# Kernel optimization log

Hardware: AMD Instinct MI355X
Metric: run time of the kernel (lower is better)

## Reference

```python
import jax, jax.numpy as jnp
import numpy as np

N = 512      # num_neurons
D = 32       # delay_dim
T = 8192     # number of sequential timesteps
OMEGA = 10.0 # base_freq
ALPHA = 0.5
DT = 1e-3    # dt_global per tick
TWO_PI = float(2.0 * np.pi)


def setup_inputs() -> dict:
    key = jax.random.key(0)
    k = jax.random.split(key, 6)
    X_real = jax.random.normal(k[0], (T, D), jnp.float32)
    X_imag = jax.random.normal(k[1], (T, D), jnp.float32)
    target_wave = jax.random.normal(k[2], (T,), jnp.float32)
    # W initialized as torch.polar(rand*0.1, rand*2pi)
    mag = jax.random.uniform(k[3], (N, D), jnp.float32) * 0.1
    ang = jax.random.uniform(k[4], (N, D), jnp.float32) * TWO_PI
    W_real = mag * jnp.cos(ang)
    W_imag = mag * jnp.sin(ang)
    phi0 = jax.random.uniform(k[5], (N,), jnp.float32) * TWO_PI
    beta0 = jnp.linspace(0.005, 0.05, N, dtype=jnp.float32)
    return {"X_real": X_real, "X_imag": X_imag, "target_wave": target_wave,
            "W_real": W_real, "W_imag": W_imag, "phi0": phi0, "beta0": beta0}


def _run(X_real, X_imag, target_wave, W_real, W_imag, phi0, beta0):
    W0 = (W_real + 1j * W_imag).astype(jnp.complex64)   # [N, D]
    X = (X_real + 1j * X_imag).astype(jnp.complex64)    # [T, D]
    lt0 = jnp.zeros((N,), jnp.float32)                  # local_time
    err0 = jnp.float32(0.0)                             # err_smooth

    def step(carry, inp):
        W, phi, beta, lt, err = carry
        x, tgt = inp                                    # x: [D] complex, tgt: scalar
        gamma = jnp.exp(-ALPHA * beta)                  # time dilation Γ  [N]
        dt_local = gamma * DT                           # [N]
        lt = lt + dt_local
        Z = W @ x                                       # X_c @ W.T -> [N] complex
        theta = OMEGA * lt + phi                        # [N]
        gate = jax.nn.relu(jnp.cos(theta - jnp.angle(Z)))
        Y = jnp.abs(Z) * gate                           # [N] real
        out = jnp.sum(Y * jnp.cos(theta))               # Re(sum Y * exp(i theta))
        # thermodynamic error feedback (sequential dependency)
        raw_err = jnp.abs(tgt - out)
        err = 0.99 * err + 0.01 * raw_err
        rel_err = err / (jnp.abs(tgt) + 0.01)
        beta_target = 3.5 * jnp.exp(-5.0 * rel_err)
        tau = jnp.where(beta_target > beta, 0.5 / (gamma + 1e-6), 0.03)
        a_s = 1.0 - jnp.exp(-DT / tau)
        beta_new = jnp.clip(beta + a_s * (beta_target - beta), 0.005, 5.0)
        # Hebbian growth / viscous decay (growth.T and decay.T directly in [N,D])
        growth_t = 0.05 * Y[:, None] * x[None, :]                 # [N, D] complex
        decay_t = (beta_new * Y ** 2)[:, None].astype(jnp.complex64) * W
        W = W + (growth_t - decay_t) * dt_local[:, None].astype(jnp.complex64)
        # phase pull: imag(tgt * exp(-i theta)) = -tgt*sin(theta) for real tgt
        phi = jnp.mod(phi + (2.0 / N) * (-tgt * jnp.sin(theta)) * dt_local, TWO_PI)
        return (W, phi, beta_new, lt, err), (out, beta_new, gamma)

    _, (outs, betas, gammas) = jax.lax.scan(
        step, (W0, phi0, beta0, lt0, err0), (X, target_wave))
    return outs, betas, gammas


def reference(X_real, X_imag, target_wave, W_real, W_imag, phi0, beta0):
    return _run(X_real, X_imag, target_wave, W_real, W_imag, phi0, beta0)
```

## Files before the change

### kernel.cpp

```cpp
#include <hip/hip_runtime.h>

#define NN 512
#define DD 32
#define TT 8192

typedef float v4f __attribute__((ext_vector_type(4)));
typedef __attribute__((address_space(3))) float lds_f;
typedef __attribute__((address_space(3))) void lds_v;
typedef const __attribute__((address_space(1))) void glb_v;

constexpr float F_OMEGA = 10.0f;
constexpr float F_DT = 1e-3f;
constexpr float F_TWO_PI = 6.28318530717958647692f;
constexpr float F_INV_TWO_PI = 0.15915494309189533577f;

__device__ __forceinline__ void barrier_lgkm() {
    asm volatile("s_waitcnt lgkmcnt(0)\n\ts_barrier" ::: "memory");
}

__device__ __forceinline__ void glds4(const float* g, lds_f* dst) {
    __builtin_amdgcn_global_load_lds((glb_v*)g, (lds_v*)dst, 4, 0, 0);
}

#define DSR128(dst, addr, off) \
    asm volatile("ds_read_b128 %0, %1 offset:" #off : "=v"(dst) : "v"(addr))
#define DSR32(dst, addr, off) \
    asm volatile("ds_read_b32 %0, %1 offset:" #off : "=v"(dst) : "v"(addr))

#define DPP_ADD(x, ctrl, rmask)                                                 \
    {                                                                           \
        int _t = __builtin_amdgcn_update_dpp(0, __float_as_int(x),              \
                                             (ctrl), (rmask), 0xf, true);       \
        (x) += __int_as_float(_t);                                              \
    }

__device__ __forceinline__ float wave_reduce_to_lane63(float x) {
    DPP_ADD(x, 0xB1, 0xf);
    DPP_ADD(x, 0x4E, 0xf);
    DPP_ADD(x, 0x141, 0xf);
    DPP_ADD(x, 0x140, 0xf);
    DPP_ADD(x, 0x142, 0xa);
    DPP_ADD(x, 0x143, 0xc);
    return x;
}

__device__ __forceinline__ float hsum4(v4f a) {
    return (a.x + a.y) + (a.z + a.w);
}

__global__ __launch_bounds__(512, 2) void deerskin(
    const float* __restrict__ Xr, const float* __restrict__ Xi,
    const float* __restrict__ Tg,
    const float* __restrict__ W0r, const float* __restrict__ W0i,
    const float* __restrict__ Phi0, const float* __restrict__ Beta0,
    float* __restrict__ outs, float* __restrict__ betas, float* __restrict__ gammas)
{
    __shared__ __align__(16) float xbuf[3][72];
    __shared__ __align__(16) float sP[16];

    const int n = threadIdx.x;
    const int lane = n & 63;
    const int wid = n >> 6;

    v4f wr4[8], wi4[8];
    {
        const v4f* wr0 = (const v4f*)(W0r + n * DD);
        const v4f* wi0 = (const v4f*)(W0i + n * DD);
#pragma unroll
        for (int j = 0; j < 8; ++j) { wr4[j] = wr0[j]; wi4[j] = wi0[j]; }
    }
    float phi = Phi0[n];
    float beta = Beta0[n];
    float lt = 0.0f;
    float err = 0.0f;

    const float* xsrc = ((lane < 32) ? Xr : Xi) + (lane & 31);

    lds_f* pcur = (lds_f*)&xbuf[0][0];
    lds_f* pnxt = (lds_f*)&xbuf[1][0];
    lds_f* pfut = (lds_f*)&xbuf[2][0];

    if (wid == 0) {
        glds4(xsrc, pcur);
        glds4(xsrc + DD, pnxt);
        if (lane == 0) {
            glds4(Tg, pcur + 64);
            glds4(Tg + 1, pnxt + 64);
        }
        asm volatile("s_waitcnt vmcnt(0)" ::: "memory");
    }
    barrier_lgkm();

    for (int t = 0; t < TT; ++t) {
        if (wid == 0) {
            int tf = t + 2; tf = (tf < TT) ? tf : (TT - 1);
            glds4(xsrc + (size_t)tf * DD, pfut);
            if (lane == 0) glds4(Tg + tf, pfut + 64);
        }

        const float gamma = __expf(-0.5f * beta);
        const float dtl = gamma * F_DT;
        lt += dtl;
        const float theta = fmaf(F_OMEGA, lt, phi);
        float rev = theta * F_INV_TWO_PI;
        rev -= floorf(rev);
        const float s = __builtin_amdgcn_sinf(rev);
        const float c = __builtin_amdgcn_cosf(rev);
        const float a_sA = 1.0f - __expf(-2.0f * F_DT * (gamma + 1e-6f));
        const float a_sB = 1.0f - __expf(-F_DT / 0.03f);

        const unsigned lcur = (unsigned)(unsigned long long)pcur;
        v4f cr[8], ci[8];
        float tgt;
        DSR128(cr[0], lcur, 0);   DSR128(cr[1], lcur, 16);
        DSR128(cr[2], lcur, 32);  DSR128(cr[3], lcur, 48);
        DSR128(cr[4], lcur, 64);  DSR128(cr[5], lcur, 80);
        DSR128(cr[6], lcur, 96);  DSR128(cr[7], lcur, 112);
        DSR128(ci[0], lcur, 128); DSR128(ci[1], lcur, 144);
        DSR128(ci[2], lcur, 160); DSR128(ci[3], lcur, 176);
        DSR128(ci[4], lcur, 192); DSR128(ci[5], lcur, 208);
        DSR128(ci[6], lcur, 224); DSR128(ci[7], lcur, 240);
        DSR32(tgt, lcur, 256);
        asm volatile("s_waitcnt lgkmcnt(0)"
            : "+v"(cr[0]), "+v"(cr[1]), "+v"(cr[2]), "+v"(cr[3]),
              "+v"(cr[4]), "+v"(cr[5]), "+v"(cr[6]), "+v"(cr[7]),
              "+v"(ci[0]), "+v"(ci[1]), "+v"(ci[2]), "+v"(ci[3]),
              "+v"(ci[4]), "+v"(ci[5]), "+v"(ci[6]), "+v"(ci[7]),
              "+v"(tgt) :: "memory");

        v4f Arr = {0,0,0,0}, Aii = {0,0,0,0}, Ari = {0,0,0,0}, Air = {0,0,0,0};
#pragma unroll
        for (int j = 0; j < 8; ++j) {
            Arr += wr4[j] * cr[j];
            Aii += wi4[j] * ci[j];
            Ari += wr4[j] * ci[j];
            Air += wi4[j] * cr[j];
        }
        const float zr = hsum4(Arr) - hsum4(Aii);
        const float zi = hsum4(Ari) + hsum4(Air);

        const float Y = fmaxf(fmaf(zr, c, zi * s), 0.0f);

        float v = wave_reduce_to_lane63(Y * c);
        if (lane == 63) sP[((t & 1) << 3) + wid] = v;

        const float inv_t = 1.0f / (fabsf(tgt) + 0.01f);
        const float yy = Y * Y;
        const float g = 0.05f * Y * dtl;
        phi += (2.0f / (float)NN) * (-tgt * s) * dtl;
        phi = phi - F_TWO_PI * floorf(phi * F_INV_TWO_PI);

        if (wid == 0) asm volatile("s_waitcnt vmcnt(5)" ::: "memory");
        barrier_lgkm();

        const float4* sp4 = (const float4*)(sP + ((t & 1) << 3));
        const float4 p0 = sp4[0], p1 = sp4[1];
        const float out = ((p0.x + p0.y) + (p0.z + p0.w)) +
                          ((p1.x + p1.y) + (p1.z + p1.w));

        const float raw = fabsf(tgt - out);
        err = 0.99f * err + 0.01f * raw;
        const float rel = err * inv_t;
        const float btg = 3.5f * __expf(-5.0f * rel);
        const float a_s = (btg > beta) ? a_sA : a_sB;
        float bnew = beta + a_s * (btg - beta);
        bnew = fminf(fmaxf(bnew, 0.005f), 5.0f);

        const float k = (bnew * yy) * dtl;
        const float m1 = 1.0f - k;
        const v4f m1v = {m1, m1, m1, m1};
        const v4f gv = {g, g, g, g};
#pragma unroll
        for (int j = 0; j < 8; ++j) {
            wr4[j] = wr4[j] * m1v + gv * cr[j];
            wi4[j] = wi4[j] * m1v + gv * ci[j];
        }

        gammas[t * NN + n] = gamma;
        betas[t * NN + n] = bnew;
        if (lane == 63) outs[t] = out;
        beta = bnew;

        lds_f* tmp = pcur; pcur = pnxt; pnxt = pfut; pfut = tmp;
    }
}

extern "C" void kernel_launch(void* const* d_in, const int* in_sizes, int n_in,
                              void* d_out, int out_size, void* d_ws, size_t ws_size,
                              hipStream_t stream) {
    const float* Xr    = (const float*)d_in[0];
    const float* Xi    = (const float*)d_in[1];
    const float* Tg    = (const float*)d_in[2];
    const float* W0r   = (const float*)d_in[3];
    const float* W0i   = (const float*)d_in[4];
    const float* Phi0  = (const float*)d_in[5];
    const float* Beta0 = (const float*)d_in[6];

    float* outs   = (float*)d_out;
    float* betas  = outs + TT;
    float* gammas = betas + (size_t)TT * NN;

    deerskin<<<1, NN, 0, stream>>>(Xr, Xi, Tg, W0r, W0i, Phi0, Beta0,
                                   outs, betas, gammas);
}
```

Measured before the change: 9.200 ms.

## Split each neuron's dot product across two threads using 1024-thread block

Each neuron is now handled by a thread pair, each owning half of the 32 delay weights, and partial complex sums are combined with a DPP swap. This halves the per-thread serial FMA chain and register footprint, and gives more waves per SIMD in the single-block sequential loop. In exchange, the per-step barrier spans 16 waves and extra reduction work is added. Scalar state (phi, beta, err) is computed redundantly on both threads of each pair.

```diff
diff --git a/kernel.cpp b/kernel.cpp
--- a/kernel.cpp
+++ b/kernel.cpp
@@ -48,7 +48,7 @@
     return (a.x + a.y) + (a.z + a.w);
 }
 
-__global__ __launch_bounds__(512, 2) void deerskin(
+__global__ __launch_bounds__(1024, 4) void deerskin(
     const float* __restrict__ Xr, const float* __restrict__ Xi,
     const float* __restrict__ Tg,
     const float* __restrict__ W0r, const float* __restrict__ W0i,
@@ -56,18 +56,20 @@
     float* __restrict__ outs, float* __restrict__ betas, float* __restrict__ gammas)
 {
     __shared__ __align__(16) float xbuf[3][72];
-    __shared__ __align__(16) float sP[16];
-
-    const int n = threadIdx.x;
-    const int lane = n & 63;
-    const int wid = n >> 6;
-
-    v4f wr4[8], wi4[8];
+    __shared__ __align__(16) float sP[32];
+
+    const int tid = threadIdx.x;
+    const int n = tid >> 1;
+    const int h = tid & 1;
+    const int lane = tid & 63;
+    const int wid = tid >> 6;
+
+    v4f wr4[4], wi4[4];
     {
-        const v4f* wr0 = (const v4f*)(W0r + n * DD);
-        const v4f* wi0 = (const v4f*)(W0i + n * DD);
+        const v4f* wr0 = (const v4f*)(W0r + n * DD + h * 16);
+        const v4f* wi0 = (const v4f*)(W0i + n * DD + h * 16);
 #pragma unroll
-        for (int j = 0; j < 8; ++j) { wr4[j] = wr0[j]; wi4[j] = wi0[j]; }
+        for (int j = 0; j < 4; ++j) { wr4[j] = wr0[j]; wi4[j] = wi0[j]; }
     }
     float phi = Phi0[n];
     float beta = Beta0[n];
@@ -110,39 +112,37 @@
         const float a_sB = 1.0f - __expf(-F_DT / 0.03f);
 
         const unsigned lcur = (unsigned)(unsigned long long)pcur;
-        v4f cr[8], ci[8];
+        const unsigned lhalf = lcur + (unsigned)(h * 64);
+        v4f cr[4], ci[4];
         float tgt;
-        DSR128(cr[0], lcur, 0);   DSR128(cr[1], lcur, 16);
-        DSR128(cr[2], lcur, 32);  DSR128(cr[3], lcur, 48);
-        DSR128(cr[4], lcur, 64);  DSR128(cr[5], lcur, 80);
-        DSR128(cr[6], lcur, 96);  DSR128(cr[7], lcur, 112);
-        DSR128(ci[0], lcur, 128); DSR128(ci[1], lcur, 144);
-        DSR128(ci[2], lcur, 160); DSR128(ci[3], lcur, 176);
-        DSR128(ci[4], lcur, 192); DSR128(ci[5], lcur, 208);
-        DSR128(ci[6], lcur, 224); DSR128(ci[7], lcur, 240);
+        DSR128(cr[0], lhalf, 0);   DSR128(cr[1], lhalf, 16);
+        DSR128(cr[2], lhalf, 32);  DSR128(cr[3], lhalf, 48);
+        DSR128(ci[0], lhalf, 128); DSR128(ci[1], lhalf, 144);
+        DSR128(ci[2], lhalf, 160); DSR128(ci[3], lhalf, 176);
         DSR32(tgt, lcur, 256);
         asm volatile("s_waitcnt lgkmcnt(0)"
             : "+v"(cr[0]), "+v"(cr[1]), "+v"(cr[2]), "+v"(cr[3]),
-              "+v"(cr[4]), "+v"(cr[5]), "+v"(cr[6]), "+v"(cr[7]),
               "+v"(ci[0]), "+v"(ci[1]), "+v"(ci[2]), "+v"(ci[3]),
-              "+v"(ci[4]), "+v"(ci[5]), "+v"(ci[6]), "+v"(ci[7]),
               "+v"(tgt) :: "memory");
 
         v4f Arr = {0,0,0,0}, Aii = {0,0,0,0}, Ari = {0,0,0,0}, Air = {0,0,0,0};
 #pragma unroll
-        for (int j = 0; j < 8; ++j) {
+        for (int j = 0; j < 4; ++j) {
             Arr += wr4[j] * cr[j];
             Aii += wi4[j] * ci[j];
             Ari += wr4[j] * ci[j];
             Air += wi4[j] * cr[j];
         }
-        const float zr = hsum4(Arr) - hsum4(Aii);
-        const float zi = hsum4(Ari) + hsum4(Air);
+        float zr = hsum4(Arr) - hsum4(Aii);
+        float zi = hsum4(Ari) + hsum4(Air);
+        DPP_ADD(zr, 0xB1, 0xf);
+        DPP_ADD(zi, 0xB1, 0xf);
 
         const float Y = fmaxf(fmaf(zr, c, zi * s), 0.0f);
 
-        float v = wave_reduce_to_lane63(Y * c);
-        if (lane == 63) sP[((t & 1) << 3) + wid] = v;
+        float v = h ? 0.0f : (Y * c);
+        v = wave_reduce_to_lane63(v);
+        if (lane == 63) sP[((t & 1) << 4) + wid] = v;
 
         const float inv_t = 1.0f / (fabsf(tgt) + 0.01f);
         const float yy = Y * Y;
@@ -153,10 +153,13 @@
         if (wid == 0) asm volatile("s_waitcnt vmcnt(5)" ::: "memory");
         barrier_lgkm();
 
-        const float4* sp4 = (const float4*)(sP + ((t & 1) << 3));
-        const float4 p0 = sp4[0], p1 = sp4[1];
-        const float out = ((p0.x + p0.y) + (p0.z + p0.w)) +
+        const float4* sp4 = (const float4*)(sP + ((t & 1) << 4));
+        const float4 p0 = sp4[0], p1 = sp4[1], p2 = sp4[2], p3 = sp4[3];
+        const float o01 = ((p0.x + p0.y) + (p0.z + p0.w)) +
                           ((p1.x + p1.y) + (p1.z + p1.w));
+        const float o23 = ((p2.x + p2.y) + (p2.z + p2.w)) +
+                          ((p3.x + p3.y) + (p3.z + p3.w));
+        const float out = o01 + o23;
 
         const float raw = fabsf(tgt - out);
         err = 0.99f * err + 0.01f * raw;
@@ -171,13 +174,15 @@
         const v4f m1v = {m1, m1, m1, m1};
         const v4f gv = {g, g, g, g};
 #pragma unroll
-        for (int j = 0; j < 8; ++j) {
+        for (int j = 0; j < 4; ++j) {
             wr4[j] = wr4[j] * m1v + gv * cr[j];
             wi4[j] = wi4[j] * m1v + gv * ci[j];
         }
 
-        gammas[t * NN + n] = gamma;
-        betas[t * NN + n] = bnew;
+        if (h == 0) {
+            gammas[t * NN + n] = gamma;
+            betas[t * NN + n] = bnew;
+        }
         if (lane == 63) outs[t] = out;
         beta = bnew;
 
@@ -200,6 +205,6 @@
     float* betas  = outs + TT;
     float* gammas = betas + (size_t)TT * NN;
 
-    deerskin<<<1, NN, 0, stream>>>(Xr, Xi, Tg, W0r, W0i, Phi0, Beta0,
-                                   outs, betas, gammas);
-}
+    deerskin<<<1, 1024, 0, stream>>>(Xr, Xi, Tg, W0r, W0i, Phi0, Beta0,
+                                     outs, betas, gammas);
+}
```

Result: slower. 11.54 ms (+25.4%).

## Load x rows directly into registers with one-step-ahead global prefetch

Applied to the files above, without the earlier changes.

Drops the LDS staging ring, where wave 0 copied each row of x and the target into LDS and every thread then read it back with ds_read. Each thread now issues broadcast global_load_dwordx4 loads for the next timestep straight into a second register set. The loop is unrolled by two so the two register sets swap roles each step. This removes the LDS round trip and wave 0's vmcnt wait ahead of the barrier. In exchange every wave issues 17 vector memory loads per step, doubles the register footprint for x, and depends on a hand-counted vmcnt(21) that assumes a fixed number of stores are in flight.

```diff
diff --git a/kernel.cpp b/kernel.cpp
--- a/kernel.cpp
+++ b/kernel.cpp
@@ -5,9 +5,6 @@
 #define TT 8192
 
 typedef float v4f __attribute__((ext_vector_type(4)));
-typedef __attribute__((address_space(3))) float lds_f;
-typedef __attribute__((address_space(3))) void lds_v;
-typedef const __attribute__((address_space(1))) void glb_v;
 
 constexpr float F_OMEGA = 10.0f;
 constexpr float F_DT = 1e-3f;
@@ -18,14 +15,14 @@
     asm volatile("s_waitcnt lgkmcnt(0)\n\ts_barrier" ::: "memory");
 }
 
-__device__ __forceinline__ void glds4(const float* g, lds_f* dst) {
-    __builtin_amdgcn_global_load_lds((glb_v*)g, (lds_v*)dst, 4, 0, 0);
-}
-
-#define DSR128(dst, addr, off) \
-    asm volatile("ds_read_b128 %0, %1 offset:" #off : "=v"(dst) : "v"(addr))
-#define DSR32(dst, addr, off) \
-    asm volatile("ds_read_b32 %0, %1 offset:" #off : "=v"(dst) : "v"(addr))
+#define GLD4M(dst, base, off) \
+    asm volatile("global_load_dwordx4 %0, %1, off offset:" #off \
+                 : "=v"(dst) : "v"(base) : "memory")
+#define GLD4(dst, base, off) \
+    asm volatile("global_load_dwordx4 %0, %1, off offset:" #off \
+                 : "=v"(dst) : "v"(base))
+#define GLD1(dst, base) \
+    asm volatile("global_load_dword %0, %1, off" : "=v"(dst) : "v"(base))
 
 #define DPP_ADD(x, ctrl, rmask)                                                 \
     {                                                                           \
@@ -48,6 +45,113 @@
     return (a.x + a.y) + (a.z + a.w);
 }
 
+__device__ __forceinline__ void issue_batch(
+    int tn, const float* Xr, const float* Xi, const float* Tg,
+    v4f (&nr)[8], v4f (&ni)[8], float& ntg)
+{
+    const unsigned long long bxr = (unsigned long long)(Xr + (size_t)tn * DD);
+    const unsigned long long bxi = (unsigned long long)(Xi + (size_t)tn * DD);
+    const unsigned long long btg = (unsigned long long)(Tg + tn);
+    GLD4M(nr[0], bxr, 0);   GLD4(nr[1], bxr, 16);
+    GLD4(nr[2], bxr, 32);   GLD4(nr[3], bxr, 48);
+    GLD4(nr[4], bxr, 64);   GLD4(nr[5], bxr, 80);
+    GLD4(nr[6], bxr, 96);   GLD4(nr[7], bxr, 112);
+    GLD4(ni[0], bxi, 0);    GLD4(ni[1], bxi, 16);
+    GLD4(ni[2], bxi, 32);   GLD4(ni[3], bxi, 48);
+    GLD4(ni[4], bxi, 64);   GLD4(ni[5], bxi, 80);
+    GLD4(ni[6], bxi, 96);   GLD4(ni[7], bxi, 112);
+    GLD1(ntg, btg);
+}
+
+#define WAIT_BATCH(cr, ci, tgt, cnt)                                            \
+    asm volatile("s_waitcnt vmcnt(" #cnt ")"                                    \
+        : "+v"(cr[0]), "+v"(cr[1]), "+v"(cr[2]), "+v"(cr[3]),                   \
+          "+v"(cr[4]), "+v"(cr[5]), "+v"(cr[6]), "+v"(cr[7]),                   \
+          "+v"(ci[0]), "+v"(ci[1]), "+v"(ci[2]), "+v"(ci[3]),                   \
+          "+v"(ci[4]), "+v"(ci[5]), "+v"(ci[6]), "+v"(ci[7]),                   \
+          "+v"(tgt) :: "memory")
+
+__device__ __forceinline__ void do_step(
+    int t,
+    const float* __restrict__ Xr, const float* __restrict__ Xi,
+    const float* __restrict__ Tg,
+    v4f (&wr4)[8], v4f (&wi4)[8],
+    v4f (&cr)[8], v4f (&ci)[8], float& tgt,
+    v4f (&nr)[8], v4f (&ni)[8], float& ntg,
+    float& phi, float& beta, float& lt, float& err,
+    float* __restrict__ outs, float* __restrict__ betas, float* __restrict__ gammas,
+    float* sP, int n, int lane, int wid)
+{
+    int tn = t + 1; tn = (tn < TT) ? tn : (TT - 1);
+    issue_batch(tn, Xr, Xi, Tg, nr, ni, ntg);
+
+    const float gamma = __expf(-0.5f * beta);
+    const float dtl = gamma * F_DT;
+    lt += dtl;
+    const float theta = fmaf(F_OMEGA, lt, phi);
+    float rev = theta * F_INV_TWO_PI;
+    rev -= floorf(rev);
+    const float s = __builtin_amdgcn_sinf(rev);
+    const float c = __builtin_amdgcn_cosf(rev);
+    const float a_sA = 1.0f - __expf(-2.0f * F_DT * (gamma + 1e-6f));
+    const float a_sB = 1.0f - __expf(-F_DT / 0.03f);
+
+    gammas[t * NN + n] = gamma;
+
+    WAIT_BATCH(cr, ci, tgt, 21);
+
+    v4f Arr = {0,0,0,0}, Aii = {0,0,0,0}, Ari = {0,0,0,0}, Air = {0,0,0,0};
+#pragma unroll
+    for (int j = 0; j < 8; ++j) {
+        Arr += wr4[j] * cr[j];
+        Aii += wi4[j] * ci[j];
+        Ari += wr4[j] * ci[j];
+        Air += wi4[j] * cr[j];
+    }
+    const float zr = hsum4(Arr) - hsum4(Aii);
+    const float zi = hsum4(Ari) + hsum4(Air);
+
+    const float Y = fmaxf(fmaf(zr, c, zi * s), 0.0f);
+
+    float v = wave_reduce_to_lane63(Y * c);
+    if (lane == 63) sP[((t & 1) << 3) + wid] = v;
+
+    const float inv_t = 1.0f / (fabsf(tgt) + 0.01f);
+    const float yy = Y * Y;
+    const float g = 0.05f * Y * dtl;
+    phi += (2.0f / (float)NN) * (-tgt * s) * dtl;
+    phi = phi - F_TWO_PI * floorf(phi * F_INV_TWO_PI);
+
+    barrier_lgkm();
+
+    const float4* sp4 = (const float4*)(sP + ((t & 1) << 3));
+    const float4 p0 = sp4[0], p1 = sp4[1];
+    const float out = ((p0.x + p0.y) + (p0.z + p0.w)) +
+                      ((p1.x + p1.y) + (p1.z + p1.w));
+
+    const float raw = fabsf(tgt - out);
+    err = 0.99f * err + 0.01f * raw;
+    const float rel = err * inv_t;
+    const float btg = 3.5f * __expf(-5.0f * rel);
+    const float a_s = (btg > beta) ? a_sA : a_sB;
+    float bnew = beta + a_s * (btg - beta);
+    bnew = fminf(fmaxf(bnew, 0.005f), 5.0f);
+
+    const float k = (bnew * yy) * dtl;
+    const float m1 = 1.0f - k;
+    const v4f m1v = {m1, m1, m1, m1};
+    const v4f gv = {g, g, g, g};
+#pragma unroll
+    for (int j = 0; j < 8; ++j) {
+        wr4[j] = wr4[j] * m1v + gv * cr[j];
+        wi4[j] = wi4[j] * m1v + gv * ci[j];
+    }
+
+    betas[t * NN + n] = bnew;
+    if (lane == 63) outs[t] = out;
+    beta = bnew;
+}
+
 __global__ __launch_bounds__(512, 2) void deerskin(
     const float* __restrict__ Xr, const float* __restrict__ Xi,
     const float* __restrict__ Tg,
@@ -55,7 +159,6 @@
     const float* __restrict__ Phi0, const float* __restrict__ Beta0,
     float* __restrict__ outs, float* __restrict__ betas, float* __restrict__ gammas)
 {
-    __shared__ __align__(16) float xbuf[3][72];
     __shared__ __align__(16) float sP[16];
 
     const int n = threadIdx.x;
@@ -74,114 +177,20 @@
     float lt = 0.0f;
     float err = 0.0f;
 
-    const float* xsrc = ((lane < 32) ? Xr : Xi) + (lane & 31);
-
-    lds_f* pcur = (lds_f*)&xbuf[0][0];
-    lds_f* pnxt = (lds_f*)&xbuf[1][0];
-    lds_f* pfut = (lds_f*)&xbuf[2][0];
-
-    if (wid == 0) {
-        glds4(xsrc, pcur);
-        glds4(xsrc + DD, pnxt);
-        if (lane == 0) {
-            glds4(Tg, pcur + 64);
-            glds4(Tg + 1, pnxt + 64);
-        }
-        asm volatile("s_waitcnt vmcnt(0)" ::: "memory");
-    }
+    v4f xa_r[8], xa_i[8], xb_r[8], xb_i[8];
+    float tgtA, tgtB;
+
+    issue_batch(0, Xr, Xi, Tg, xa_r, xa_i, tgtA);
+    WAIT_BATCH(xa_r, xa_i, tgtA, 0);
     barrier_lgkm();
 
-    for (int t = 0; t < TT; ++t) {
-        if (wid == 0) {
-            int tf = t + 2; tf = (tf < TT) ? tf : (TT - 1);
-            glds4(xsrc + (size_t)tf * DD, pfut);
-            if (lane == 0) glds4(Tg + tf, pfut + 64);
-        }
-
-        const float gamma = __expf(-0.5f * beta);
-        const float dtl = gamma * F_DT;
-        lt += dtl;
-        const float theta = fmaf(F_OMEGA, lt, phi);
-        float rev = theta * F_INV_TWO_PI;
-        rev -= floorf(rev);
-        const float s = __builtin_amdgcn_sinf(rev);
-        const float c = __builtin_amdgcn_cosf(rev);
-        const float a_sA = 1.0f - __expf(-2.0f * F_DT * (gamma + 1e-6f));
-        const float a_sB = 1.0f - __expf(-F_DT / 0.03f);
-
-        const unsigned lcur = (unsigned)(unsigned long long)pcur;
-        v4f cr[8], ci[8];
-        float tgt;
-        DSR128(cr[0], lcur, 0);   DSR128(cr[1], lcur, 16);
-        DSR128(cr[2], lcur, 32);  DSR128(cr[3], lcur, 48);
-        DSR128(cr[4], lcur, 64);  DSR128(cr[5], lcur, 80);
-        DSR128(cr[6], lcur, 96);  DSR128(cr[7], lcur, 112);
-        DSR128(ci[0], lcur, 128); DSR128(ci[1], lcur, 144);
-        DSR128(ci[2], lcur, 160); DSR128(ci[3], lcur, 176);
-        DSR128(ci[4], lcur, 192); DSR128(ci[5], lcur, 208);
-        DSR128(ci[6], lcur, 224); DSR128(ci[7], lcur, 240);
-        DSR32(tgt, lcur, 256);
-        asm volatile("s_waitcnt lgkmcnt(0)"
-            : "+v"(cr[0]), "+v"(cr[1]), "+v"(cr[2]), "+v"(cr[3]),
-              "+v"(cr[4]), "+v"(cr[5]), "+v"(cr[6]), "+v"(cr[7]),
-              "+v"(ci[0]), "+v"(ci[1]), "+v"(ci[2]), "+v"(ci[3]),
-              "+v"(ci[4]), "+v"(ci[5]), "+v"(ci[6]), "+v"(ci[7]),
-              "+v"(tgt) :: "memory");
-
-        v4f Arr = {0,0,0,0}, Aii = {0,0,0,0}, Ari = {0,0,0,0}, Air = {0,0,0,0};
-#pragma unroll
-        for (int j = 0; j < 8; ++j) {
-            Arr += wr4[j] * cr[j];
-            Aii += wi4[j] * ci[j];
-            Ari += wr4[j] * ci[j];
-            Air += wi4[j] * cr[j];
-        }
-        const float zr = hsum4(Arr) - hsum4(Aii);
-        const float zi = hsum4(Ari) + hsum4(Air);
-
-        const float Y = fmaxf(fmaf(zr, c, zi * s), 0.0f);
-
-        float v = wave_reduce_to_lane63(Y * c);
-        if (lane == 63) sP[((t & 1) << 3) + wid] = v;
-
-        const float inv_t = 1.0f / (fabsf(tgt) + 0.01f);
-        const float yy = Y * Y;
-        const float g = 0.05f * Y * dtl;
-        phi += (2.0f / (float)NN) * (-tgt * s) * dtl;
-        phi = phi - F_TWO_PI * floorf(phi * F_INV_TWO_PI);
-
-        if (wid == 0) asm volatile("s_waitcnt vmcnt(5)" ::: "memory");
-        barrier_lgkm();
-
-        const float4* sp4 = (const float4*)(sP + ((t & 1) << 3));
-        const float4 p0 = sp4[0], p1 = sp4[1];
-        const float out = ((p0.x + p0.y) + (p0.z + p0.w)) +
-                          ((p1.x + p1.y) + (p1.z + p1.w));
-
-        const float raw = fabsf(tgt - out);
-        err = 0.99f * err + 0.01f * raw;
-        const float rel = err * inv_t;
-        const float btg = 3.5f * __expf(-5.0f * rel);
-        const float a_s = (btg > beta) ? a_sA : a_sB;
-        float bnew = beta + a_s * (btg - beta);
-        bnew = fminf(fmaxf(bnew, 0.005f), 5.0f);
-
-        const float k = (bnew * yy) * dtl;
-        const float m1 = 1.0f - k;
-        const v4f m1v = {m1, m1, m1, m1};
-        const v4f gv = {g, g, g, g};
-#pragma unroll
-        for (int j = 0; j < 8; ++j) {
-            wr4[j] = wr4[j] * m1v + gv * cr[j];
-            wi4[j] = wi4[j] * m1v + gv * ci[j];
-        }
-
-        gammas[t * NN + n] = gamma;
-        betas[t * NN + n] = bnew;
-        if (lane == 63) outs[t] = out;
-        beta = bnew;
-
-        lds_f* tmp = pcur; pcur = pnxt; pnxt = pfut; pfut = tmp;
+    for (int t = 0; t < TT; t += 2) {
+        do_step(t,     Xr, Xi, Tg, wr4, wi4,
+                xa_r, xa_i, tgtA, xb_r, xb_i, tgtB,
+                phi, beta, lt, err, outs, betas, gammas, sP, n, lane, wid);
+        do_step(t + 1, Xr, Xi, Tg, wr4, wi4,
+                xb_r, xb_i, tgtB, xa_r, xa_i, tgtA,
+                phi, beta, lt, err, outs, betas, gammas, sP, n, lane, wid);
     }
 }
 
```

Result: slower. 12.15 ms (+32.1%).

## Load x once per lane and broadcast via readlane, prefetching next step

Applied to the files above, without the earlier changes.

Instead of every lane reading all 64 x values from LDS with 16 broadcast ds_read_b128 ops, each lane reads one value and the wave uses v_readlane into SGPRs to build the operand vectors. The next timestep's x and target are read right after the barrier, so the LDS latency overlaps with the error/beta update and W update. Math switches from v4f to v2f ops to suit packed-FMA with scalar operands. This cuts LDS bandwidth and VGPR pressure but adds 64 readlane instructions per step, which may serialize on the scalar path.

```diff
diff --git a/kernel.cpp b/kernel.cpp
--- a/kernel.cpp
+++ b/kernel.cpp
@@ -4,7 +4,7 @@
 #define DD 32
 #define TT 8192
 
-typedef float v4f __attribute__((ext_vector_type(4)));
+typedef float v2f __attribute__((ext_vector_type(2)));
 typedef __attribute__((address_space(3))) float lds_f;
 typedef __attribute__((address_space(3))) void lds_v;
 typedef const __attribute__((address_space(1))) void glb_v;
@@ -22,10 +22,10 @@
     __builtin_amdgcn_global_load_lds((glb_v*)g, (lds_v*)dst, 4, 0, 0);
 }
 
-#define DSR128(dst, addr, off) \
-    asm volatile("ds_read_b128 %0, %1 offset:" #off : "=v"(dst) : "v"(addr))
 #define DSR32(dst, addr, off) \
     asm volatile("ds_read_b32 %0, %1 offset:" #off : "=v"(dst) : "v"(addr))
+#define WAIT2(a, b) \
+    asm volatile("s_waitcnt lgkmcnt(0)" : "+v"(a), "+v"(b) :: "memory")
 
 #define DPP_ADD(x, ctrl, rmask)                                                 \
     {                                                                           \
@@ -44,8 +44,15 @@
     return x;
 }
 
-__device__ __forceinline__ float hsum4(v4f a) {
-    return (a.x + a.y) + (a.z + a.w);
+__device__ __forceinline__ void unpack_readlane(float vx, v2f (&xr)[16], v2f (&xi)[16]) {
+    const int vxi = __float_as_int(vx);
+#pragma unroll
+    for (int j = 0; j < 16; ++j) {
+        xr[j] = v2f{__int_as_float(__builtin_amdgcn_readlane(vxi, 2 * j)),
+                    __int_as_float(__builtin_amdgcn_readlane(vxi, 2 * j + 1))};
+        xi[j] = v2f{__int_as_float(__builtin_amdgcn_readlane(vxi, 32 + 2 * j)),
+                    __int_as_float(__builtin_amdgcn_readlane(vxi, 32 + 2 * j + 1))};
+    }
 }
 
 __global__ __launch_bounds__(512, 2) void deerskin(
@@ -62,12 +69,12 @@
     const int lane = n & 63;
     const int wid = n >> 6;
 
-    v4f wr4[8], wi4[8];
+    v2f wr[16], wi[16];
     {
-        const v4f* wr0 = (const v4f*)(W0r + n * DD);
-        const v4f* wi0 = (const v4f*)(W0i + n * DD);
-#pragma unroll
-        for (int j = 0; j < 8; ++j) { wr4[j] = wr0[j]; wi4[j] = wi0[j]; }
+        const v2f* wr0 = (const v2f*)(W0r + n * DD);
+        const v2f* wi0 = (const v2f*)(W0i + n * DD);
+#pragma unroll
+        for (int j = 0; j < 16; ++j) { wr[j] = wr0[j]; wi[j] = wi0[j]; }
     }
     float phi = Phi0[n];
     float beta = Beta0[n];
@@ -79,6 +86,9 @@
     lds_f* pcur = (lds_f*)&xbuf[0][0];
     lds_f* pnxt = (lds_f*)&xbuf[1][0];
     lds_f* pfut = (lds_f*)&xbuf[2][0];
+
+    v2f xr[16], xi[16];
+    float tgt;
 
     if (wid == 0) {
         glds4(xsrc, pcur);
@@ -90,6 +100,15 @@
         asm volatile("s_waitcnt vmcnt(0)" ::: "memory");
     }
     barrier_lgkm();
+    {
+        const unsigned lcur = (unsigned)(unsigned long long)pcur;
+        float vx, vtg;
+        DSR32(vx, lcur + 4u * (unsigned)lane, 0);
+        DSR32(vtg, lcur, 256);
+        WAIT2(vx, vtg);
+        unpack_readlane(vx, xr, xi);
+        tgt = vtg;
+    }
 
     for (int t = 0; t < TT; ++t) {
         if (wid == 0) {
@@ -109,35 +128,16 @@
         const float a_sA = 1.0f - __expf(-2.0f * F_DT * (gamma + 1e-6f));
         const float a_sB = 1.0f - __expf(-F_DT / 0.03f);
 
-        const unsigned lcur = (unsigned)(unsigned long long)pcur;
-        v4f cr[8], ci[8];
-        float tgt;
-        DSR128(cr[0], lcur, 0);   DSR128(cr[1], lcur, 16);
-        DSR128(cr[2], lcur, 32);  DSR128(cr[3], lcur, 48);
-        DSR128(cr[4], lcur, 64);  DSR128(cr[5], lcur, 80);
-        DSR128(cr[6], lcur, 96);  DSR128(cr[7], lcur, 112);
-        DSR128(ci[0], lcur, 128); DSR128(ci[1], lcur, 144);
-        DSR128(ci[2], lcur, 160); DSR128(ci[3], lcur, 176);
-        DSR128(ci[4], lcur, 192); DSR128(ci[5], lcur, 208);
-        DSR128(ci[6], lcur, 224); DSR128(ci[7], lcur, 240);
-        DSR32(tgt, lcur, 256);
-        asm volatile("s_waitcnt lgkmcnt(0)"
-            : "+v"(cr[0]), "+v"(cr[1]), "+v"(cr[2]), "+v"(cr[3]),
-              "+v"(cr[4]), "+v"(cr[5]), "+v"(cr[6]), "+v"(cr[7]),
-              "+v"(ci[0]), "+v"(ci[1]), "+v"(ci[2]), "+v"(ci[3]),
-              "+v"(ci[4]), "+v"(ci[5]), "+v"(ci[6]), "+v"(ci[7]),
-              "+v"(tgt) :: "memory");
-
-        v4f Arr = {0,0,0,0}, Aii = {0,0,0,0}, Ari = {0,0,0,0}, Air = {0,0,0,0};
-#pragma unroll
-        for (int j = 0; j < 8; ++j) {
-            Arr += wr4[j] * cr[j];
-            Aii += wi4[j] * ci[j];
-            Ari += wr4[j] * ci[j];
-            Air += wi4[j] * cr[j];
-        }
-        const float zr = hsum4(Arr) - hsum4(Aii);
-        const float zi = hsum4(Ari) + hsum4(Air);
+        v2f Arr = {0.f,0.f}, Aii = {0.f,0.f}, Ari = {0.f,0.f}, Air = {0.f,0.f};
+#pragma unroll
+        for (int j = 0; j < 16; ++j) {
+            Arr += wr[j] * xr[j];
+            Aii += wi[j] * xi[j];
+            Ari += wr[j] * xi[j];
+            Air += wi[j] * xr[j];
+        }
+        const float zr = (Arr.x + Arr.y) - (Aii.x + Aii.y);
+        const float zi = (Ari.x + Ari.y) + (Air.x + Air.y);
 
         const float Y = fmaxf(fmaf(zr, c, zi * s), 0.0f);
 
@@ -152,6 +152,13 @@
 
         if (wid == 0) asm volatile("s_waitcnt vmcnt(5)" ::: "memory");
         barrier_lgkm();
+
+        float vx, vtg;
+        {
+            const unsigned lnxt = (unsigned)(unsigned long long)pnxt;
+            DSR32(vx, lnxt + 4u * (unsigned)lane, 0);
+            DSR32(vtg, lnxt, 256);
+        }
 
         const float4* sp4 = (const float4*)(sP + ((t & 1) << 3));
         const float4 p0 = sp4[0], p1 = sp4[1];
@@ -168,18 +175,22 @@
 
         const float k = (bnew * yy) * dtl;
         const float m1 = 1.0f - k;
-        const v4f m1v = {m1, m1, m1, m1};
-        const v4f gv = {g, g, g, g};
-#pragma unroll
-        for (int j = 0; j < 8; ++j) {
-            wr4[j] = wr4[j] * m1v + gv * cr[j];
-            wi4[j] = wi4[j] * m1v + gv * ci[j];
+        const v2f m1v = {m1, m1};
+        const v2f gv = {g, g};
+#pragma unroll
+        for (int j = 0; j < 16; ++j) {
+            wr[j] = wr[j] * m1v + gv * xr[j];
+            wi[j] = wi[j] * m1v + gv * xi[j];
         }
 
         gammas[t * NN + n] = gamma;
         betas[t * NN + n] = bnew;
         if (lane == 63) outs[t] = out;
         beta = bnew;
+
+        WAIT2(vx, vtg);
+        unpack_readlane(vx, xr, xi);
+        tgt = vtg;
 
         lds_f* tmp = pcur; pcur = pnxt; pnxt = pfut; pfut = tmp;
     }
```

New measurement: 10.05 ms. +9.2%, slower.
